# Performance work log

Measured on AMD Instinct MI355X. Metric: run time of the kernel, lower is better.

The kernel has to match this reference:

```python
import jax, jax.numpy as jnp
import numpy as np

GRID = 32
N_NODES = GRID * GRID          # 1024
PATCH = 1
C_IN = 3
NODE_F = C_IN * PATCH * PATCH  # 3
HID = 256
N_CLASSES = 10


def _build_norm_adj():
    # 5-point grid stencil + self loops, symmetrically normalized: D^-1/2 A D^-1/2
    adj = np.zeros((N_NODES, N_NODES), dtype=np.float32)
    idx = np.arange(N_NODES)
    i, j = idx // GRID, idx % GRID
    adj[idx, idx] = 1.0
    for di, dj in [(-1, 0), (1, 0), (0, -1), (0, 1)]:
        ni, nj = i + di, j + dj
        ok = (ni >= 0) & (ni < GRID) & (nj >= 0) & (nj < GRID)
        adj[idx[ok], (ni * GRID + nj)[ok]] = 1.0
    deg = adj.sum(axis=1)
    dis = np.where(deg > 0, deg ** -0.5, 0.0).astype(np.float32)
    return jnp.asarray(dis[:, None] * adj * dis[None, :])


def _image_to_graph(x):
    # [B,C,H,W] -> [B, grid, patch, grid, patch] blocks -> [B, N, C*patch^2]
    B = x.shape[0]
    x = x.reshape(B, C_IN, GRID, PATCH, GRID, PATCH)
    x = jnp.transpose(x, (0, 2, 4, 1, 3, 5))
    return x.reshape(B, N_NODES, NODE_F)


def setup_inputs() -> dict:
    key = jax.random.key(0)
    ks = jax.random.split(key, 10)
    s = 0.05
    return {
        "x": jax.random.normal(ks[0], (256, 3, 32, 32), dtype=jnp.float32),
        "W1": jax.random.normal(ks[1], (HID, NODE_F), dtype=jnp.float32) * s,
        "b1": jnp.zeros((HID,), dtype=jnp.float32),
        "W2": jax.random.normal(ks[2], (HID, HID), dtype=jnp.float32) * s,
        "b2": jnp.zeros((HID,), dtype=jnp.float32),
        "W3": jax.random.normal(ks[3], (HID // 2, HID), dtype=jnp.float32) * s,
        "b3": jnp.zeros((HID // 2,), dtype=jnp.float32),
        "Wc": jax.random.normal(ks[4], (N_CLASSES, N_NODES * (HID // 2)), dtype=jnp.float32) * s,
        "bc": jnp.zeros((N_CLASSES,), dtype=jnp.float32),
        "adj": _build_norm_adj(),
    }


def _gc(h, W, b, adj):
    # Linear, then fixed-adjacency aggregation, then ReLU
    h = jnp.einsum('bnf,hf->bnh', h, W) + b
    h = jnp.einsum('mn,bnh->bmh', adj, h)
    return jax.nn.relu(h)


def reference(x, W1, b1, W2, b2, W3, b3, Wc, bc, adj):
    h = _image_to_graph(x)                 # [B, N, 3]
    h = _gc(h, W1, b1, adj)                # [B, N, 256]
    h = _gc(h, W2, b2, adj)                # [B, N, 256]
    h = _gc(h, W3, b3, adj)                # [B, N, 128]
    h = h.reshape(h.shape[0], -1)          # [B, N*128]
    return h @ Wc.T + bc                   # [B, 10]
```

## Files before the change

kernel.cpp:

```cpp
#include <hip/hip_runtime.h>
#include <stdint.h>

#define N_NODES 1024
#define NCLS 10
#define KDIM 131072

typedef unsigned short u16;
typedef __bf16 bf16x8 __attribute__((ext_vector_type(8)));
typedef float f32x4 __attribute__((ext_vector_type(4)));

__device__ __forceinline__ float b2f_lo(uint32_t u) {
  union { float f; uint32_t u; } v; v.u = u << 16; return v.f;
}
__device__ __forceinline__ float b2f_hi(uint32_t u) {
  union { float f; uint32_t u; } v; v.u = u & 0xFFFF0000u; return v.f;
}
__device__ __forceinline__ u16 f2b(float f) {
  union { float f; uint32_t u; } v; v.f = f;
  uint32_t r = v.u + 0x7FFF + ((v.u >> 16) & 1);
  return (u16)(r >> 16);
}
__device__ __forceinline__ uint32_t pkbf(float a, float b) {
#if __has_builtin(__builtin_amdgcn_cvt_pk_bf16_f32)
  typedef __bf16 bf2 __attribute__((ext_vector_type(2)));
  bf2 r = __builtin_amdgcn_cvt_pk_bf16_f32(a, b);
  union { bf2 v; uint32_t u; } c; c.v = r; return c.u;
#else
  union { float f; uint32_t u; } va, vb; va.f = a; vb.f = b;
  uint32_t ra = (va.u + 0x7FFF + ((va.u >> 16) & 1)) >> 16;
  uint32_t rb = (vb.u + 0x7FFF + ((vb.u >> 16) & 1)) & 0xFFFF0000u;
  return ra | rb;
#endif
}

__device__ __forceinline__ void async_copy16(const u16* g, u16* l) {
  __builtin_amdgcn_global_load_lds(
      (const __attribute__((address_space(1))) void*)g,
      (__attribute__((address_space(3))) void*)l, 16, 0, 0);
}

__device__ __forceinline__ void agg8(const u16* p, float c, float2* acc) {
  uint4 v = *(const uint4*)p;
  const uint32_t* u = (const uint32_t*)&v;
#pragma unroll
  for (int e = 0; e < 4; e++) {
    acc[e].x += c * b2f_lo(u[e]);
    acc[e].y += c * b2f_hi(u[e]);
  }
}

__global__ __launch_bounds__(256) void cvt_w_kernel(const float* __restrict__ w,
                                                    u16* __restrict__ o, int n) {
  int i = blockIdx.x * 256 + threadIdx.x;
  if (i < n) o[i] = f2b(w[i]);
}

__global__ __launch_bounds__(256) void prep_wc_kernel(const float* __restrict__ wc,
                                                      u16* __restrict__ o) {
  int i = blockIdx.x * 256 + threadIdx.x;
  int row = i >> 17;
  int col = i & (KDIM - 1);
  o[i] = (row < NCLS) ? f2b(wc[row * KDIM + col]) : (u16)0;
}

__global__ __launch_bounds__(256) void prep_tab_kernel(const float* __restrict__ adj,
                                                       int* __restrict__ nbi,
                                                       float* __restrict__ nbc,
                                                       float* __restrict__ r) {
  int m = blockIdx.x * 256 + threadIdx.x;
  if (m >= N_NODES) return;
  int i = m >> 5, j = m & 31;
  const float* arow = adj + (size_t)m * N_NODES;
  int n[5]; float c[5];
  n[0] = m;                      c[0] = arow[m];
  n[1] = (i > 0)  ? m - 32 : m;  c[1] = (i > 0)  ? arow[m - 32] : 0.f;
  n[2] = (i < 31) ? m + 32 : m;  c[2] = (i < 31) ? arow[m + 32] : 0.f;
  n[3] = (j > 0)  ? m - 1  : m;  c[3] = (j > 0)  ? arow[m - 1]  : 0.f;
  n[4] = (j < 31) ? m + 1  : m;  c[4] = (j < 31) ? arow[m + 1]  : 0.f;
  float s = 0.f;
#pragma unroll
  for (int t = 0; t < 5; t++) { nbi[m * 5 + t] = n[t]; nbc[m * 5 + t] = c[t]; s += c[t]; }
  r[m] = s;
}

__global__ __launch_bounds__(256) void outinit_kernel(const float* __restrict__ bc,
                                                      float* __restrict__ out) {
  int idx = blockIdx.x * 256 + threadIdx.x;
  if (idx < 256 * NCLS) out[idx] = bc[idx % NCLS];
}

__global__ __launch_bounds__(256) void l1agg_kernel(
    const float* __restrict__ x,
    const float* __restrict__ W1,
    const float* __restrict__ b1,
    const int* __restrict__ nbi, const float* __restrict__ nbc,
    const float* __restrict__ r,
    u16* __restrict__ g)
{
  __shared__ u16 h1s[128 * 256];
  __shared__ float gxs[128][4];
  __shared__ float W1s[768];
  __shared__ float b1s[256];
  int p0 = blockIdx.x * 64;
  int b = p0 >> 10;
  int m0 = p0 & 1023;
  int e0 = m0 - 32;
  int tid = threadIdx.x;

  b1s[tid] = b1[tid];
  for (int i = tid; i < 768; i += 256) W1s[i] = W1[i];

  if (tid < 128) {
    int n = e0 + tid;
    float g0 = 0.f, g1 = 0.f, g2 = 0.f, rn = 0.f;
    if (n >= 0 && n < N_NODES) {
      const float* xb = x + (size_t)b * 3072;
#pragma unroll
      for (int t = 0; t < 5; t++) {
        int nb = nbi[n * 5 + t]; float cf = nbc[n * 5 + t];
        g0 += cf * xb[nb];
        g1 += cf * xb[1024 + nb];
        g2 += cf * xb[2048 + nb];
      }
      rn = r[n];
    }
    gxs[tid][0] = g0; gxs[tid][1] = g1; gxs[tid][2] = g2; gxs[tid][3] = rn;
  }
  __syncthreads();

  int ch8 = (tid & 31) * 8;
  float w[8][3], bb[8];
#pragma unroll
  for (int c = 0; c < 8; c++) {
    w[c][0] = W1s[(ch8 + c) * 3];
    w[c][1] = W1s[(ch8 + c) * 3 + 1];
    w[c][2] = W1s[(ch8 + c) * 3 + 2];
    bb[c] = b1s[ch8 + c];
  }

#pragma unroll
  for (int it = 0; it < 16; it++) {
    int node = (tid >> 5) + it * 8;
    float g0 = gxs[node][0], g1 = gxs[node][1], g2 = gxs[node][2], rn = gxs[node][3];
    uint32_t pk[4];
#pragma unroll
    for (int c = 0; c < 8; c += 2) {
      float z0 = fmaxf(g0 * w[c][0] + g1 * w[c][1] + g2 * w[c][2] + rn * bb[c], 0.f);
      float z1 = fmaxf(g0 * w[c+1][0] + g1 * w[c+1][1] + g2 * w[c+1][2] + rn * bb[c+1], 0.f);
      pk[c >> 1] = pkbf(z0, z1);
    }
    *(uint4*)&h1s[node * 256 + ch8] = *(uint4*)pk;
  }
  __syncthreads();

#pragma unroll
  for (int it = 0; it < 8; it++) {
    int node = (tid >> 5) + it * 8;
    int m = m0 + node;
    float2 acc[4] = {};
#pragma unroll
    for (int t = 0; t < 5; t++) {
      int nb = nbi[m * 5 + t]; float cf = nbc[m * 5 + t];
      agg8(&h1s[(nb - e0) * 256 + ch8], cf, acc);
    }
    uint4 o;
    o.x = pkbf(acc[0].x, acc[0].y); o.y = pkbf(acc[1].x, acc[1].y);
    o.z = pkbf(acc[2].x, acc[2].y); o.w = pkbf(acc[3].x, acc[3].y);
    *(uint4*)&g[(size_t)(p0 + node) * 256 + ch8] = o;
  }
}

__global__ __launch_bounds__(256) void mm_kernel(
    const u16* __restrict__ A, const u16* __restrict__ W,
    const float* __restrict__ bias, const float* __restrict__ r,
    u16* __restrict__ C, int N)
{
  const int K = 256;
  __shared__ u16 As[4 * 128 * 64];
  __shared__ u16 Bs[4 * 128 * 64];
  int n0 = blockIdx.x * 128;
  int m0 = blockIdx.y * 128;
  int tid = threadIdx.x;
  int w = tid >> 6, l = tid & 63;
  int wm = w >> 1, wn = w & 1;

  int r8 = l >> 3, oct = l & 7;
  int so = (oct ^ r8) << 3;
  const u16* ga0 = A + (size_t)(m0 + w * 32 + r8) * K + so;
  const u16* gb0 = W + (size_t)(n0 + w * 32 + r8) * K + so;

#pragma unroll
  for (int kg = 0; kg < 4; kg++)
#pragma unroll
    for (int q = 0; q < 4; q++) {
      async_copy16(ga0 + (size_t)q * 8 * K + kg * 64, &As[kg * 8192 + (w * 32 + q * 8) * 64]);
      async_copy16(gb0 + (size_t)q * 8 * K + kg * 64, &Bs[kg * 8192 + (w * 32 + q * 8) * 64]);
    }

  f32x4 acc[4][4] = {};
  int lrow = l & 15, lq = l >> 4;
  int s = lrow & 7;
  __syncthreads();

#pragma unroll
  for (int kq = 0; kq < 8; kq++) {
    int kg = kq >> 1, kh = kq & 1;
    int po = (((kh << 2) | lq) ^ s) << 3;
    bf16x8 af[4], bf[4];
#pragma unroll
    for (int t = 0; t < 4; t++) {
      af[t] = *(const bf16x8*)(&As[kg * 8192 + (wm * 64 + t * 16 + lrow) * 64 + po]);
      bf[t] = *(const bf16x8*)(&Bs[kg * 8192 + (wn * 64 + t * 16 + lrow) * 64 + po]);
    }
#pragma unroll
    for (int mt = 0; mt < 4; mt++)
#pragma unroll
      for (int nt = 0; nt < 4; nt++)
        acc[mt][nt] = __builtin_amdgcn_mfma_f32_16x16x32_bf16(af[mt], bf[nt], acc[mt][nt], 0, 0, 0);
  }

#pragma unroll
  for (int mt = 0; mt < 4; mt++)
#pragma unroll
    for (int nt = 0; nt < 4; nt++) {
      f32x4 v = acc[mt][nt];
      int col = n0 + wn * 64 + nt * 16 + lrow;
      float bs = bias[col];
#pragma unroll
      for (int i2 = 0; i2 < 4; i2++) {
        int row = m0 + wm * 64 + mt * 16 + lq * 4 + i2;
        float val = v[i2] + r[row & 1023] * bs;
        C[(size_t)row * N + col] = f2b(fmaxf(val, 0.f));
      }
    }
}

__global__ __launch_bounds__(256) void mm3agg_kernel(
    const u16* __restrict__ H,
    const u16* __restrict__ W,
    const float* __restrict__ bias, const float* __restrict__ r,
    const int* __restrict__ nbi, const float* __restrict__ nbc,
    u16* __restrict__ C)
{
  const int K = 256, N = 128;
  const int AST = 264;
  __shared__ u16 As[128 * AST];
  __shared__ u16 Bs[4 * 128 * 64];
  int m0 = blockIdx.x * 128;
  int tid = threadIdx.x;
  int w = tid >> 6, l = tid & 63;
  int wm = w >> 1, wn = w & 1;

  int r8 = l >> 3, oct = l & 7;
  int so = (oct ^ r8) << 3;
  const u16* gb0 = W + (size_t)(w * 32 + r8) * K + so;
#pragma unroll
  for (int kg = 0; kg < 4; kg++)
#pragma unroll
    for (int q = 0; q < 4; q++)
      async_copy16(gb0 + (size_t)q * 8 * K + kg * 64, &Bs[kg * 8192 + (w * 32 + q * 8) * 64]);

  {
    int arow = tid >> 1;
    int acol0 = (tid & 1) * 128;
    int pg = m0 + arow;
    int node = pg & 1023;
    const u16* hb = H + ((size_t)(pg >> 10) << 10) * 256 + acol0;
    const u16* nbp[5]; float cf[5];
#pragma unroll
    for (int j = 0; j < 5; j++) {
      nbp[j] = hb + (size_t)nbi[node * 5 + j] * 256;
      cf[j] = nbc[node * 5 + j];
    }
    u16* dst = &As[arow * AST + acol0];
#pragma unroll 4
    for (int u = 0; u < 16; u++) {
      float2 acc[4] = {};
#pragma unroll
      for (int j = 0; j < 5; j++) agg8(nbp[j] + u * 8, cf[j], acc);
      uint4 o;
      o.x = pkbf(acc[0].x, acc[0].y); o.y = pkbf(acc[1].x, acc[1].y);
      o.z = pkbf(acc[2].x, acc[2].y); o.w = pkbf(acc[3].x, acc[3].y);
      *(uint4*)(dst + u * 8) = o;
    }
  }

  f32x4 acc[4][4] = {};
  int lrow = l & 15, lq = l >> 4;
  int s = lrow & 7;
  __syncthreads();

  const u16* pa = &As[(wm * 64 + lrow) * AST];
#pragma unroll
  for (int kq = 0; kq < 8; kq++) {
    int kg = kq >> 1, kh = kq & 1;
    int po = (((kh << 2) | lq) ^ s) << 3;
    bf16x8 af[4], bf[4];
#pragma unroll
    for (int t = 0; t < 4; t++) {
      af[t] = *(const bf16x8*)(pa + t * 16 * AST + kq * 32 + lq * 8);
      bf[t] = *(const bf16x8*)(&Bs[kg * 8192 + (wn * 64 + t * 16 + lrow) * 64 + po]);
    }
#pragma unroll
    for (int mt = 0; mt < 4; mt++)
#pragma unroll
      for (int nt = 0; nt < 4; nt++)
        acc[mt][nt] = __builtin_amdgcn_mfma_f32_16x16x32_bf16(af[mt], bf[nt], acc[mt][nt], 0, 0, 0);
  }

#pragma unroll
  for (int mt = 0; mt < 4; mt++)
#pragma unroll
    for (int nt = 0; nt < 4; nt++) {
      f32x4 v = acc[mt][nt];
      int col = wn * 64 + nt * 16 + lrow;
      float bs = bias[col];
#pragma unroll
      for (int i2 = 0; i2 < 4; i2++) {
        int row = m0 + wm * 64 + mt * 16 + lq * 4 + i2;
        float val = v[i2] + r[row & 1023] * bs;
        C[(size_t)row * N + col] = f2b(fmaxf(val, 0.f));
      }
    }
}

__global__ __launch_bounds__(256) void cls_kernel(
    const u16* __restrict__ h3,
    const u16* __restrict__ Wcb,
    float* __restrict__ out,
    int b0)
{
  int mt = blockIdx.x;
  int split = blockIdx.y;
  int w = threadIdx.x >> 6, l = threadIdx.x & 63;
  int lrow = l & 15, lq = l >> 4;
  f32x4 acc = {};
  int kbase = split * 4096 + w * 1024;
  const u16* pa = h3 + (size_t)(mt * 16 + lrow) * KDIM + kbase + lq * 8;
  const u16* pb = Wcb + (size_t)lrow * KDIM + kbase + lq * 8;
#pragma unroll 4
  for (int kk = 0; kk < 1024; kk += 32) {
    bf16x8 a = *(const bf16x8*)(pa + kk);
    bf16x8 b = *(const bf16x8*)(pb + kk);
    acc = __builtin_amdgcn_mfma_f32_16x16x32_bf16(a, b, acc, 0, 0, 0);
  }
  if (lrow < NCLS) {
#pragma unroll
    for (int i2 = 0; i2 < 4; i2++) {
      int b = b0 + mt * 16 + lq * 4 + i2;
      atomicAdd(&out[b * NCLS + lrow], acc[i2]);
    }
  }
}

extern "C" void kernel_launch(void* const* d_in, const int* in_sizes, int n_in,
                              void* d_out, int out_size, void* d_ws, size_t ws_size,
                              hipStream_t stream) {
  const float* x   = (const float*)d_in[0];
  const float* W1  = (const float*)d_in[1];
  const float* b1  = (const float*)d_in[2];
  const float* W2  = (const float*)d_in[3];
  const float* b2  = (const float*)d_in[4];
  const float* W3  = (const float*)d_in[5];
  const float* b3  = (const float*)d_in[6];
  const float* Wc  = (const float*)d_in[7];
  const float* bc  = (const float*)d_in[8];
  const float* adj = (const float*)d_in[9];
  float* out = (float*)d_out;
  const int B = 256;

  uint8_t* ws = (uint8_t*)d_ws;
  u16* W2b = (u16*)ws;  ws += (size_t)256 * 256 * 2;
  u16* W3b = (u16*)ws;  ws += (size_t)128 * 256 * 2;
  u16* Wcb = (u16*)ws;  ws += (size_t)16 * KDIM * 2;
  float* rr  = (float*)ws; ws += 1024 * 4;
  int*   nbi = (int*)ws;   ws += 1024 * 5 * 4;
  float* nbc = (float*)ws; ws += 1024 * 5 * 4;
  uintptr_t al = ((uintptr_t)ws + 255) & ~(uintptr_t)255;
  ws = (uint8_t*)al;
  size_t used = (size_t)(ws - (uint8_t*)d_ws);
  size_t avail = (ws_size > used) ? ws_size - used : 0;
  int chunk = 256;
  while (chunk > 32 && (size_t)chunk * 1024 * 256 * 2 * 2 > avail) chunk >>= 1;
  u16* bufA = (u16*)ws;
  u16* bufB = bufA + (size_t)chunk * 1024 * 256;

  cvt_w_kernel<<<256, 256, 0, stream>>>(W2, W2b, 256 * 256);
  cvt_w_kernel<<<128, 256, 0, stream>>>(W3, W3b, 128 * 256);
  prep_wc_kernel<<<(16 * KDIM) / 256, 256, 0, stream>>>(Wc, Wcb);
  prep_tab_kernel<<<4, 256, 0, stream>>>(adj, nbi, nbc, rr);
  outinit_kernel<<<(256 * NCLS + 255) / 256, 256, 0, stream>>>(bc, out);

  for (int b0 = 0; b0 < B; b0 += chunk) {
    const float* xb = x + (size_t)b0 * 3 * 1024;
    int M = chunk * 1024;
    l1agg_kernel<<<M / 64, 256, 0, stream>>>(xb, W1, b1, nbi, nbc, rr, bufB);
    {
      dim3 g(2, M / 128);
      mm_kernel<<<g, 256, 0, stream>>>(bufB, W2b, b2, rr, bufA, 256);
    }
    mm3agg_kernel<<<M / 128, 256, 0, stream>>>(bufA, W3b, b3, rr, nbi, nbc, bufB);
    dim3 gc(chunk / 16, 32);
    cls_kernel<<<gc, 256, 0, stream>>>(bufB, Wcb, out, b0);
  }
}
```

Baseline: 430.0 us.

## Double-buffer K chunks in GEMM kernels and overlap aggregation with MFMA

Both GEMM kernels stop staging the full 256-wide K dimension in LDS before computing. They now stream 64-wide K chunks through two LDS buffers, issuing the next chunk's async copies before computing on the current one. In mm3agg_kernel, the neighbour-gather loads for the next chunk are issued before the MFMA loop and aggregated into the spare buffer afterwards, so that global latency hides behind matrix math. The smaller LDS footprint plus launch_bounds(256,2) aims for two resident blocks per CU, in exchange for more barriers per tile and extra register pressure from holding the gathered tiles.

Measured after the change: 349.6 us. -18.7%, faster.

```diff
diff --git a/kernel.cpp b/kernel.cpp
--- a/kernel.cpp
+++ b/kernel.cpp
@@ -39,8 +39,7 @@
       (__attribute__((address_space(3))) void*)l, 16, 0, 0);
 }
 
-__device__ __forceinline__ void agg8(const u16* p, float c, float2* acc) {
-  uint4 v = *(const uint4*)p;
+__device__ __forceinline__ void agg8(uint4 v, float c, float2* acc) {
   const uint32_t* u = (const uint32_t*)&v;
 #pragma unroll
   for (int e = 0; e < 4; e++) {
@@ -161,7 +160,7 @@
 #pragma unroll
     for (int t = 0; t < 5; t++) {
       int nb = nbi[m * 5 + t]; float cf = nbc[m * 5 + t];
-      agg8(&h1s[(nb - e0) * 256 + ch8], cf, acc);
+      agg8(*(const uint4*)&h1s[(nb - e0) * 256 + ch8], cf, acc);
     }
     uint4 o;
     o.x = pkbf(acc[0].x, acc[0].y); o.y = pkbf(acc[1].x, acc[1].y);
@@ -170,14 +169,14 @@
   }
 }
 
-__global__ __launch_bounds__(256) void mm_kernel(
+__global__ __launch_bounds__(256, 2) void mm_kernel(
     const u16* __restrict__ A, const u16* __restrict__ W,
     const float* __restrict__ bias, const float* __restrict__ r,
     u16* __restrict__ C, int N)
 {
   const int K = 256;
-  __shared__ u16 As[4 * 128 * 64];
-  __shared__ u16 Bs[4 * 128 * 64];
+  __shared__ u16 As[2][128 * 64];
+  __shared__ u16 Bs[2][128 * 64];
   int n0 = blockIdx.x * 128;
   int m0 = blockIdx.y * 128;
   int tid = threadIdx.x;
@@ -189,35 +188,42 @@
   const u16* ga0 = A + (size_t)(m0 + w * 32 + r8) * K + so;
   const u16* gb0 = W + (size_t)(n0 + w * 32 + r8) * K + so;
 
-#pragma unroll
-  for (int kg = 0; kg < 4; kg++)
-#pragma unroll
-    for (int q = 0; q < 4; q++) {
-      async_copy16(ga0 + (size_t)q * 8 * K + kg * 64, &As[kg * 8192 + (w * 32 + q * 8) * 64]);
-      async_copy16(gb0 + (size_t)q * 8 * K + kg * 64, &Bs[kg * 8192 + (w * 32 + q * 8) * 64]);
-    }
+#define MM_ISSUE(kq, buf) \
+  _Pragma("unroll") for (int q = 0; q < 4; q++) { \
+    async_copy16(ga0 + (size_t)q * 8 * K + (kq) * 64, &As[buf][(w * 32 + q * 8) * 64]); \
+    async_copy16(gb0 + (size_t)q * 8 * K + (kq) * 64, &Bs[buf][(w * 32 + q * 8) * 64]); \
+  }
+
+  MM_ISSUE(0, 0);
 
   f32x4 acc[4][4] = {};
   int lrow = l & 15, lq = l >> 4;
   int s = lrow & 7;
-  __syncthreads();
-
-#pragma unroll
-  for (int kq = 0; kq < 8; kq++) {
-    int kg = kq >> 1, kh = kq & 1;
-    int po = (((kh << 2) | lq) ^ s) << 3;
-    bf16x8 af[4], bf[4];
-#pragma unroll
-    for (int t = 0; t < 4; t++) {
-      af[t] = *(const bf16x8*)(&As[kg * 8192 + (wm * 64 + t * 16 + lrow) * 64 + po]);
-      bf[t] = *(const bf16x8*)(&Bs[kg * 8192 + (wn * 64 + t * 16 + lrow) * 64 + po]);
-    }
-#pragma unroll
-    for (int mt = 0; mt < 4; mt++)
-#pragma unroll
-      for (int nt = 0; nt < 4; nt++)
-        acc[mt][nt] = __builtin_amdgcn_mfma_f32_16x16x32_bf16(af[mt], bf[nt], acc[mt][nt], 0, 0, 0);
-  }
+
+#pragma unroll
+  for (int kq = 0; kq < 4; kq++) {
+    int buf = kq & 1;
+    __syncthreads();
+    if (kq < 3) MM_ISSUE(kq + 1, buf ^ 1);
+    const u16* pa = &As[buf][(wm * 64 + lrow) * 64];
+    const u16* pb = &Bs[buf][(wn * 64 + lrow) * 64];
+#pragma unroll
+    for (int kh = 0; kh < 2; kh++) {
+      int po = (((kh << 2) | lq) ^ s) << 3;
+      bf16x8 af[4], bf[4];
+#pragma unroll
+      for (int t = 0; t < 4; t++) {
+        af[t] = *(const bf16x8*)(pa + t * 16 * 64 + po);
+        bf[t] = *(const bf16x8*)(pb + t * 16 * 64 + po);
+      }
+#pragma unroll
+      for (int mt = 0; mt < 4; mt++)
+#pragma unroll
+        for (int nt = 0; nt < 4; nt++)
+          acc[mt][nt] = __builtin_amdgcn_mfma_f32_16x16x32_bf16(af[mt], bf[nt], acc[mt][nt], 0, 0, 0);
+    }
+  }
+#undef MM_ISSUE
 
 #pragma unroll
   for (int mt = 0; mt < 4; mt++)
@@ -235,7 +241,7 @@
     }
 }
 
-__global__ __launch_bounds__(256) void mm3agg_kernel(
+__global__ __launch_bounds__(256, 2) void mm3agg_kernel(
     const u16* __restrict__ H,
     const u16* __restrict__ W,
     const float* __restrict__ bias, const float* __restrict__ r,
@@ -243,70 +249,89 @@
     u16* __restrict__ C)
 {
   const int K = 256, N = 128;
-  const int AST = 264;
-  __shared__ u16 As[128 * AST];
-  __shared__ u16 Bs[4 * 128 * 64];
+  const int AST = 72;
+  __shared__ u16 As[2][128 * AST];
+  __shared__ u16 Bs[2][128 * 64];
   int m0 = blockIdx.x * 128;
   int tid = threadIdx.x;
   int w = tid >> 6, l = tid & 63;
   int wm = w >> 1, wn = w & 1;
 
+  int arow = tid >> 1;
+  int acol = (tid & 1) * 32;
+  int pg = m0 + arow;
+  int node = pg & 1023;
+  const u16* hb = H + ((size_t)(pg >> 10) << 10) * 256 + acol;
+  const u16* nbp[5]; float cf[5];
+#pragma unroll
+  for (int j = 0; j < 5; j++) {
+    nbp[j] = hb + (size_t)nbi[node * 5 + j] * 256;
+    cf[j] = nbc[node * 5 + j];
+  }
+
   int r8 = l >> 3, oct = l & 7;
   int so = (oct ^ r8) << 3;
   const u16* gb0 = W + (size_t)(w * 32 + r8) * K + so;
-#pragma unroll
-  for (int kg = 0; kg < 4; kg++)
-#pragma unroll
-    for (int q = 0; q < 4; q++)
-      async_copy16(gb0 + (size_t)q * 8 * K + kg * 64, &Bs[kg * 8192 + (w * 32 + q * 8) * 64]);
-
-  {
-    int arow = tid >> 1;
-    int acol0 = (tid & 1) * 128;
-    int pg = m0 + arow;
-    int node = pg & 1023;
-    const u16* hb = H + ((size_t)(pg >> 10) << 10) * 256 + acol0;
-    const u16* nbp[5]; float cf[5];
-#pragma unroll
-    for (int j = 0; j < 5; j++) {
-      nbp[j] = hb + (size_t)nbi[node * 5 + j] * 256;
-      cf[j] = nbc[node * 5 + j];
-    }
-    u16* dst = &As[arow * AST + acol0];
-#pragma unroll 4
-    for (int u = 0; u < 16; u++) {
-      float2 acc[4] = {};
-#pragma unroll
-      for (int j = 0; j < 5; j++) agg8(nbp[j] + u * 8, cf[j], acc);
-      uint4 o;
-      o.x = pkbf(acc[0].x, acc[0].y); o.y = pkbf(acc[1].x, acc[1].y);
-      o.z = pkbf(acc[2].x, acc[2].y); o.w = pkbf(acc[3].x, acc[3].y);
-      *(uint4*)(dst + u * 8) = o;
-    }
-  }
+
+#define M3_ISSUEB(kq, buf) \
+  _Pragma("unroll") for (int q = 0; q < 4; q++) \
+    async_copy16(gb0 + (size_t)q * 8 * K + (kq) * 64, &Bs[buf][(w * 32 + q * 8) * 64]);
+
+#define M3_LOADA(kq) \
+  _Pragma("unroll") for (int j = 0; j < 5; j++) \
+    _Pragma("unroll") for (int q = 0; q < 4; q++) \
+      L[j][q] = *(const uint4*)(nbp[j] + (kq) * 64 + q * 8);
+
+#define M3_AGGSTORE(buf) { \
+  u16* dst = &As[buf][arow * AST + acol]; \
+  _Pragma("unroll") for (int q = 0; q < 4; q++) { \
+    float2 acc2[4] = {}; \
+    _Pragma("unroll") for (int j = 0; j < 5; j++) agg8(L[j][q], cf[j], acc2); \
+    uint4 o; \
+    o.x = pkbf(acc2[0].x, acc2[0].y); o.y = pkbf(acc2[1].x, acc2[1].y); \
+    o.z = pkbf(acc2[2].x, acc2[2].y); o.w = pkbf(acc2[3].x, acc2[3].y); \
+    *(uint4*)(dst + q * 8) = o; \
+  } }
+
+  uint4 L[5][4];
+  M3_ISSUEB(0, 0);
+  M3_LOADA(0);
+  M3_AGGSTORE(0);
 
   f32x4 acc[4][4] = {};
   int lrow = l & 15, lq = l >> 4;
   int s = lrow & 7;
-  __syncthreads();
-
-  const u16* pa = &As[(wm * 64 + lrow) * AST];
-#pragma unroll
-  for (int kq = 0; kq < 8; kq++) {
-    int kg = kq >> 1, kh = kq & 1;
-    int po = (((kh << 2) | lq) ^ s) << 3;
-    bf16x8 af[4], bf[4];
-#pragma unroll
-    for (int t = 0; t < 4; t++) {
-      af[t] = *(const bf16x8*)(pa + t * 16 * AST + kq * 32 + lq * 8);
-      bf[t] = *(const bf16x8*)(&Bs[kg * 8192 + (wn * 64 + t * 16 + lrow) * 64 + po]);
-    }
-#pragma unroll
-    for (int mt = 0; mt < 4; mt++)
-#pragma unroll
-      for (int nt = 0; nt < 4; nt++)
-        acc[mt][nt] = __builtin_amdgcn_mfma_f32_16x16x32_bf16(af[mt], bf[nt], acc[mt][nt], 0, 0, 0);
-  }
+
+#pragma unroll
+  for (int kq = 0; kq < 4; kq++) {
+    int buf = kq & 1;
+    __syncthreads();
+    if (kq < 3) {
+      M3_ISSUEB(kq + 1, buf ^ 1);
+      M3_LOADA(kq + 1);
+    }
+    const u16* pa = &As[buf][(wm * 64 + lrow) * AST];
+    const u16* pb = &Bs[buf][(wn * 64 + lrow) * 64];
+#pragma unroll
+    for (int kh = 0; kh < 2; kh++) {
+      int po = (((kh << 2) | lq) ^ s) << 3;
+      bf16x8 af[4], bf[4];
+#pragma unroll
+      for (int t = 0; t < 4; t++) {
+        af[t] = *(const bf16x8*)(pa + t * 16 * AST + kh * 32 + lq * 8);
+        bf[t] = *(const bf16x8*)(pb + t * 16 * 64 + po);
+      }
+#pragma unroll
+      for (int mt = 0; mt < 4; mt++)
+#pragma unroll
+        for (int nt = 0; nt < 4; nt++)
+          acc[mt][nt] = __builtin_amdgcn_mfma_f32_16x16x32_bf16(af[mt], bf[nt], acc[mt][nt], 0, 0, 0);
+    }
+    if (kq < 3) M3_AGGSTORE(buf ^ 1);
+  }
+#undef M3_ISSUEB
+#undef M3_LOADA
+#undef M3_AGGSTORE
 
 #pragma unroll
   for (int mt = 0; mt < 4; mt++)
```
